# Kernel optimization log

Hardware: AMD Instinct MI355X
Metric: run time of the kernel (lower is better)

The kernel has to match this reference:

```python
import jax, jax.numpy as jnp
import numpy as np

B, N = 8, 2048
DIN, DS, DO, GE, HID = 2, 32, 32, 8, 32
CHEB_K = 3
N_SUPPORTS = 2
D_CAT = DIN + 2 * DS            # 66, input to the two AGCNs
D_BASIS = N_SUPPORTS * CHEB_K * D_CAT  # 396


def setup_inputs() -> dict:
    key = jax.random.key(0)
    ks = jax.random.split(key, 12)
    xt = jax.random.normal(ks[0], (B, N, DIN), dtype=jnp.float32)
    state1 = jax.random.normal(ks[1], (B, N, DS), dtype=jnp.float32)
    state2 = jax.random.normal(ks[2], (B, N, DS), dtype=jnp.float32)
    gatembedding = jax.random.normal(ks[3], (B, N, GE), dtype=jnp.float32)
    # adaptive adjacency supports: row-stochastic (softmax over neighbors), 2 supports
    supports = jax.nn.softmax(jax.random.normal(ks[4], (N_SUPPORTS, B, N, N), dtype=jnp.float32), axis=-1)

    def xavier(k, shape):
        fan_in, fan_out = shape[0], shape[1]
        std = float(np.sqrt(2.0 / (fan_in + fan_out)))
        return jax.random.normal(k, shape, dtype=jnp.float32) * std

    return {
        "xt": xt, "state1": state1, "state2": state2,
        "gatembedding": gatembedding, "supports": supports,
        "mlp_w": xavier(ks[5], (DIN + 2 * DS + GE, DO)), "mlp_b": jnp.zeros((DO,), jnp.float32),
        "gate_w": xavier(ks[6], (D_BASIS, 3 * DO)), "gate_b": jnp.zeros((3 * DO,), jnp.float32),
        "upd_w": xavier(ks[7], (D_BASIS, DO)), "upd_b": jnp.zeros((DO,), jnp.float32),
        "hop_w": xavier(ks[8], (DO, HID)), "hop_b": jnp.zeros((HID,), jnp.float32),
    }


def _agcn(x, supports, W, b):
    """Chebyshev graph conv: for each support, basis T0=I, T1=A, Tk=2A Tk-1 - Tk-2,
    applied to x (linearity lets us recurse on T_k @ x directly, same math)."""
    terms = []
    for i in range(N_SUPPORTS):  # fixed small structural loop
        A = supports[i]                                  # [B,N,N]
        t_prev, t_cur = x, jnp.einsum('bnm,bmc->bnc', A, x)
        ts = [t_prev, t_cur]
        for _ in range(2, CHEB_K):
            t_prev, t_cur = t_cur, 2.0 * jnp.einsum('bnm,bmc->bnc', A, t_cur) - t_prev
            ts.append(t_cur)
        terms.extend(ts)
    x_g = jnp.concatenate(terms, axis=-1)                # [B,N,2*K*c]
    return jnp.einsum('bni,io->bno', x_g, W) + b


def reference(xt, state1, state2, gatembedding, supports,
              mlp_w, mlp_b, gate_w, gate_b, upd_w, upd_b, hop_w, hop_b):
    # MLP mixing gate between the two incoming states
    gate_in = jnp.concatenate([xt, state1, state2, gatembedding], axis=-1)
    mr = jax.nn.sigmoid(gate_in @ mlp_w + mlp_b)
    state = mr * state1 + (1.0 - mr) * state2
    # graph-conv GRU gates
    X = jnp.concatenate([xt, state1, state2], axis=-1)   # [B,N,DIN+2*DS]
    zz_r = jax.nn.sigmoid(_agcn(X, supports, gate_w, gate_b))
    z1, z2, r = zz_r[..., :DO], zz_r[..., DO:2 * DO], zz_r[..., 2 * DO:]
    candidate = jnp.concatenate([xt, z1 * state1, z2 * state2], axis=-1)
    hc = jnp.tanh(_agcn(candidate, supports, upd_w, upd_b))
    h = r * state + (1.0 - r) * hc                        # [B,N,DO]
    transnext = h @ hop_w + hop_b                         # [B,N,HID]
    return (h, transnext)
```

## Files before the change

### kernel.cpp

```cpp
#include <hip/hip_runtime.h>

#define NN 2048
#define BB 8
#define KT 416
#define SLOT (80 * NN)

typedef __bf16 bf16;
typedef __bf16 bf16x4 __attribute__((ext_vector_type(4)));
typedef __bf16 bf16x8 __attribute__((ext_vector_type(8)));
typedef float  f32x4  __attribute__((ext_vector_type(4)));

__device__ __forceinline__ void bar_lgkm() {
    asm volatile("s_waitcnt lgkmcnt(0)" ::: "memory");
    __builtin_amdgcn_s_barrier();
}

__global__ void prep_weights(const float* __restrict__ gw, const float* __restrict__ uw,
                             bf16* __restrict__ Wg, bf16* __restrict__ Wu)
{
    int i = blockIdx.x * 256 + threadIdx.x;
    if (i < 96 * KT) {
        int o = i / KT, k = i % KT, t = k / 80, c = k % 80;
        float v = 0.0f;
        if (c < 66) {
            if (t == 0)      v = gw[c*96+o] - gw[(132+c)*96+o] + gw[(198+c)*96+o] - gw[(330+c)*96+o];
            else if (t == 1) v = gw[(66+c)*96+o];
            else if (t == 2) v = 2.0f * gw[(132+c)*96+o];
            else if (t == 3) v = gw[(264+c)*96+o];
            else             v = 2.0f * gw[(330+c)*96+o];
        }
        Wg[i] = (bf16)v;
    }
    if (i < 32 * KT) {
        int o = i / KT, k = i % KT, t = k / 80, c = k % 80;
        float v = 0.0f;
        if (c < 66) {
            if (t == 0)      v = uw[c*32+o] - uw[(132+c)*32+o] + uw[(198+c)*32+o] - uw[(330+c)*32+o];
            else if (t == 1) v = uw[(66+c)*32+o];
            else if (t == 2) v = 2.0f * uw[(132+c)*32+o];
            else if (t == 3) v = uw[(264+c)*32+o];
            else             v = 2.0f * uw[(330+c)*32+o];
        }
        Wu[i] = (bf16)v;
    }
}

__global__ __launch_bounds__(256)
void prep_nodes(const float* __restrict__ xt, const float* __restrict__ s1,
                const float* __restrict__ s2, const float* __restrict__ ge,
                const float* __restrict__ mlp_w, const float* __restrict__ mlp_b,
                float* __restrict__ state, bf16* __restrict__ T)
{
    __shared__ float wl[74 * 32];
    __shared__ float bl[32];
    __shared__ __align__(16) float statel[64][36];
    __shared__ __align__(16) bf16  Xl[80][72];
    const int tid = threadIdx.x;

    for (int i = tid; i < 592; i += 256) ((float4*)wl)[i] = ((const float4*)mlp_w)[i];
    if (tid < 32) bl[tid] = mlp_b[tid];
    {
        int bb = blockIdx.x >> 5, chunk = blockIdx.x & 31;
        uint2* dst = (uint2*)((char*)T + ((size_t)bb * KT * NN + 400 * NN) * 2 + (size_t)chunk * 2048);
        dst[tid] = make_uint2(0u, 0u);
    }
    for (int i = tid; i < 14 * 64; i += 256) Xl[66 + (i >> 6)][i & 63] = (bf16)0.0f;
    __syncthreads();

    const int nl = tid & 63, og = tid >> 6, o0 = og * 8;
    const size_t node0 = (size_t)blockIdx.x * 64;
    const size_t node = node0 + nl;
    const int b = (int)(node0 >> 11);
    const int nb0 = (int)(node0 & 2047);
    const float* p1 = s1 + node * 32;
    const float* p2 = s2 + node * 32;
    const float* pg = ge + node * 8;

    float acc[8];
    #pragma unroll
    for (int j = 0; j < 8; ++j) acc[j] = bl[o0 + j];
    float2 px = *(const float2*)(xt + node * 2);
    #pragma unroll
    for (int j = 0; j < 8; ++j) acc[j] += px.x * wl[o0 + j] + px.y * wl[32 + o0 + j];

    float k1[8], k2[8];
    #pragma unroll
    for (int ii = 0; ii < 8; ++ii) {
        float4 v = *(const float4*)(p1 + ii * 4);
        const float* vp = (const float*)&v;
        if (ii == 2 * og)     { k1[0]=vp[0]; k1[1]=vp[1]; k1[2]=vp[2]; k1[3]=vp[3]; }
        if (ii == 2 * og + 1) { k1[4]=vp[0]; k1[5]=vp[1]; k1[6]=vp[2]; k1[7]=vp[3]; }
        #pragma unroll
        for (int p = 0; p < 4; ++p) {
            #pragma unroll
            for (int j = 0; j < 8; ++j) acc[j] += vp[p] * wl[(2 + ii*4 + p) * 32 + o0 + j];
        }
    }
    #pragma unroll
    for (int ii = 0; ii < 8; ++ii) {
        float4 v = *(const float4*)(p2 + ii * 4);
        const float* vp = (const float*)&v;
        if (ii == 2 * og)     { k2[0]=vp[0]; k2[1]=vp[1]; k2[2]=vp[2]; k2[3]=vp[3]; }
        if (ii == 2 * og + 1) { k2[4]=vp[0]; k2[5]=vp[1]; k2[6]=vp[2]; k2[7]=vp[3]; }
        #pragma unroll
        for (int p = 0; p < 4; ++p) {
            #pragma unroll
            for (int j = 0; j < 8; ++j) acc[j] += vp[p] * wl[(34 + ii*4 + p) * 32 + o0 + j];
        }
    }
    #pragma unroll
    for (int ii = 0; ii < 2; ++ii) {
        float4 v = *(const float4*)(pg + ii * 4);
        const float* vp = (const float*)&v;
        #pragma unroll
        for (int p = 0; p < 4; ++p) {
            #pragma unroll
            for (int j = 0; j < 8; ++j) acc[j] += vp[p] * wl[(66 + ii*4 + p) * 32 + o0 + j];
        }
    }
    #pragma unroll
    for (int j = 0; j < 8; ++j) {
        float mr = 1.0f / (1.0f + __expf(-acc[j]));
        statel[nl][o0 + j] = mr * k1[j] + (1.0f - mr) * k2[j];
        Xl[2 + o0 + j][nl]  = (bf16)k1[j];
        Xl[34 + o0 + j][nl] = (bf16)k2[j];
    }
    if (og == 0) { Xl[0][nl] = (bf16)px.x; Xl[1][nl] = (bf16)px.y; }
    __syncthreads();

    for (int i = tid; i < 512; i += 256) {
        int n_ = i >> 3, c = (i & 7) * 4;
        *(float4*)&state[node0 * 32 + n_ * 32 + c] = *(const float4*)&statel[n_][c];
    }
    bf16* Tb = T + (size_t)b * KT * NN;
    for (int i = tid; i < 640; i += 256) {
        int r = i >> 3, seg = i & 7;
        *(uint4*)(Tb + (size_t)r * NN + nb0 + seg * 8) = *(const uint4*)&Xl[r][seg * 8];
    }
}

template<int MODE>
__global__ __launch_bounds__(256, 2)
void gemm_cheb(const float* __restrict__ Aall, bf16* Abf, bf16* T,
               int in0, int in1, int out0, int out1)
{
    __shared__ __align__(16) bf16 lA[2][64][40];
    __shared__ __align__(16) bf16 lB[2][80][40];

    const int sb = blockIdx.y;
    const int s = sb >> 3, b = sb & 7;
    const int m0 = blockIdx.x * 64;
    const float* A = Aall + (size_t)sb * NN * NN + (size_t)m0 * NN;
    bf16* Ab = Abf + (size_t)sb * NN * NN + (size_t)m0 * NN;
    bf16* Tb = T + (size_t)b * KT * NN;
    const bf16* Bt = Tb + (size_t)(s ? in1 : in0) * SLOT;
    bf16*       Ct = Tb + (size_t)(s ? out1 : out0) * SLOT + m0;

    const int tid  = threadIdx.x;
    const int wave = tid >> 6;
    const int lane = tid & 63;

    const int arow = tid >> 3, aseg = tid & 7;
    const int arw2 = tid >> 2, asg2 = tid & 3;
    const int brow = tid >> 2, bseg = tid & 3;
    const int brow2 = 64 + (tid >> 2);

    float4 ra0A, ra1A, ra0B, ra1B;
    uint4  ra2A, ra2B;
    uint4  rb0A, rb1A, rb0B, rb1B;

    auto gload = [&](float4& xa0, float4& xa1, uint4& xa2, uint4& xb0, uint4& xb1, int k0) {
        if constexpr (MODE == 2) {
            xa2 = *(const uint4*)(Ab + (size_t)arw2 * NN + k0 + asg2 * 8);
        } else {
            xa0 = *(const float4*)(A + (size_t)arow * NN + k0 + aseg * 4);
            xa1 = *(const float4*)(A + (size_t)(arow + 32) * NN + k0 + aseg * 4);
        }
        xb0 = *(const uint4*)(Bt + (size_t)brow * NN + k0 + bseg * 8);
        if (tid < 64) xb1 = *(const uint4*)(Bt + (size_t)brow2 * NN + k0 + bseg * 8);
    };
    auto stage = [&](int buf, float4& xa0, float4& xa1, uint4& xa2, uint4& xb0, uint4& xb1, int k0) {
        if constexpr (MODE == 2) {
            *(uint4*)&lA[buf][arw2][asg2 * 8] = xa2;
        } else {
            bf16x4 a0, a1;
            a0[0]=(bf16)xa0.x; a0[1]=(bf16)xa0.y; a0[2]=(bf16)xa0.z; a0[3]=(bf16)xa0.w;
            a1[0]=(bf16)xa1.x; a1[1]=(bf16)xa1.y; a1[2]=(bf16)xa1.z; a1[3]=(bf16)xa1.w;
            *(bf16x4*)&lA[buf][arow][aseg * 4]      = a0;
            *(bf16x4*)&lA[buf][arow + 32][aseg * 4] = a1;
            if constexpr (MODE == 1) {
                *(bf16x4*)(Ab + (size_t)arow * NN + k0 + aseg * 4)        = a0;
                *(bf16x4*)(Ab + (size_t)(arow + 32) * NN + k0 + aseg * 4) = a1;
            }
        }
        *(uint4*)&lB[buf][brow][bseg * 8] = xb0;
        if (tid < 64) *(uint4*)&lB[buf][brow2][bseg * 8] = xb1;
    };

    f32x4 acc[5] = {};
    const int frow = lane & 15;
    const int fko  = (lane >> 4) * 8;

    auto compute = [&](int buf) {
        bf16x8 af = *(const bf16x8*)&lA[buf][wave * 16 + frow][fko];
        #pragma unroll
        for (int ct = 0; ct < 5; ++ct) {
            bf16x8 bv = *(const bf16x8*)&lB[buf][ct * 16 + frow][fko];
            acc[ct] = __builtin_amdgcn_mfma_f32_16x16x32_bf16(af, bv, acc[ct], 0, 0, 0);
        }
    };

    gload(ra0A, ra1A, ra2A, rb0A, rb1A, 0);
    gload(ra0B, ra1B, ra2B, rb0B, rb1B, 32);
    for (int kt = 0; kt < 64; kt += 2) {
        stage(0, ra0A, ra1A, ra2A, rb0A, rb1A, kt * 32);
        if (kt < 62) gload(ra0A, ra1A, ra2A, rb0A, rb1A, (kt + 2) * 32);
        bar_lgkm();
        compute(0);
        stage(1, ra0B, ra1B, ra2B, rb0B, rb1B, (kt + 1) * 32);
        if (kt < 61) gload(ra0B, ra1B, ra2B, rb0B, rb1B, (kt + 3) * 32);
        bar_lgkm();
        compute(1);
    }

    const int ccol = lane & 15;
    const int crow = (lane >> 4) * 4;
    #pragma unroll
    for (int ct = 0; ct < 5; ++ct) {
        bf16x4 o;
        o[0]=(bf16)acc[ct][0]; o[1]=(bf16)acc[ct][1]; o[2]=(bf16)acc[ct][2]; o[3]=(bf16)acc[ct][3];
        *(bf16x4*)&Ct[(size_t)(ct * 16 + ccol) * NN + wave * 16 + crow] = o;
    }
}

__global__ __launch_bounds__(256)
void proj_gate(const bf16* T, const bf16* __restrict__ Wg, const float* __restrict__ gate_b,
               const float* __restrict__ s1, const float* __restrict__ s2,
               bf16* Tmut, float* __restrict__ rT)
{
    __shared__ __align__(16) bf16 Wl[96][424];
    __shared__ __align__(16) bf16 Bl[2][64][44];
    const int b = blockIdx.y, n0 = blockIdx.x * 64, tid = threadIdx.x;
    const bf16* Tb = T + (size_t)b * KT * NN;

    for (int i = tid; i < 96 * 52; i += 256) {
        int r = i / 52, seg = i % 52;
        *(uint4*)&Wl[r][seg * 8] = *(const uint4*)(Wg + (size_t)r * KT + seg * 8);
    }
    const int kk = tid >> 3, seg = tid & 7;
    uint4 rbA, rbB;
    auto gloadv = [&](uint4& r, int k0) { r = *(const uint4*)(Tb + (size_t)(k0 + kk) * NN + n0 + seg * 8); };
    auto scat = [&](int buf, uint4& r) {
        bf16 tmp[8]; *(uint4*)tmp = r;
        #pragma unroll
        for (int j = 0; j < 8; ++j) Bl[buf][seg * 8 + j][kk] = tmp[j];
    };
    const int lane = tid & 63, wave = tid >> 6;
    const int fr = lane & 15, qd = lane >> 4;

    f32x4 acc[6] = {};
    auto comp = [&](int buf, int st) {
        bf16x8 bv = *(const bf16x8*)&Bl[buf][wave * 16 + fr][qd * 8];
        #pragma unroll
        for (int f = 0; f < 6; ++f) {
            bf16x8 av = *(const bf16x8*)&Wl[f * 16 + fr][st * 32 + qd * 8];
            acc[f] = __builtin_amdgcn_mfma_f32_16x16x32_bf16(av, bv, acc[f], 0, 0, 0);
        }
    };

    gloadv(rbA, 0); gloadv(rbB, 32);
    for (int st = 0; st < 12; st += 2) {
        scat(0, rbA);
        gloadv(rbA, (st + 2) * 32);
        bar_lgkm();
        comp(0, st);
        scat(1, rbB);
        if (st < 10) gloadv(rbB, (st + 3) * 32);
        bar_lgkm();
        comp(1, st + 1);
    }
    scat(0, rbA);
    bar_lgkm();
    comp(0, 12);

    const int nn = n0 + wave * 16 + fr;
    const size_t node = (size_t)b * NN + nn;
    bf16* Cd = Tmut + (size_t)b * KT * NN;
    #pragma unroll
    for (int f = 0; f < 6; ++f) {
        const int o0 = f * 16 + qd * 4;
        float4 gb4 = *(const float4*)(gate_b + o0);
        const float* gb = (const float*)&gb4;
        float sg[4];
        #pragma unroll
        for (int r = 0; r < 4; ++r) sg[r] = 1.0f / (1.0f + __expf(-(acc[f][r] + gb[r])));
        if (f < 2) {
            float4 sv4 = *(const float4*)(s1 + node * 32 + o0);
            const float* sv = (const float*)&sv4;
            #pragma unroll
            for (int r = 0; r < 4; ++r) Cd[(size_t)(2 + o0 + r) * NN + nn] = (bf16)(sg[r] * sv[r]);
        } else if (f < 4) {
            const int oo = o0 - 32;
            float4 sv4 = *(const float4*)(s2 + node * 32 + oo);
            const float* sv = (const float*)&sv4;
            #pragma unroll
            for (int r = 0; r < 4; ++r) Cd[(size_t)(34 + oo + r) * NN + nn] = (bf16)(sg[r] * sv[r]);
        } else {
            const int oo = o0 - 64;
            #pragma unroll
            for (int r = 0; r < 4; ++r) rT[((size_t)b * 32 + oo + r) * NN + nn] = sg[r];
        }
    }
}

__global__ __launch_bounds__(256)
void proj_upd(const bf16* __restrict__ T, const bf16* __restrict__ Wu,
              const float* __restrict__ upd_b, const float* __restrict__ state,
              const float* __restrict__ rT, const float* __restrict__ hop_w,
              const float* __restrict__ hop_b, float* __restrict__ out)
{
    __shared__ __align__(16) bf16 Wl[32][424];
    __shared__ __align__(16) bf16 Bl[2][64][44];
    __shared__ __align__(16) float hsh[64][36];
    __shared__ float hw[1024];
    const int b = blockIdx.y, n0 = blockIdx.x * 64, tid = threadIdx.x;
    const bf16* Tb = T + (size_t)b * KT * NN;

    for (int i = tid; i < 32 * 52; i += 256) {
        int r = i / 52, seg = i % 52;
        *(uint4*)&Wl[r][seg * 8] = *(const uint4*)(Wu + (size_t)r * KT + seg * 8);
    }
    for (int i = tid; i < 256; i += 256) ((float4*)hw)[i] = ((const float4*)hop_w)[i];
    const int kk = tid >> 3, seg = tid & 7;
    uint4 rbA, rbB;
    auto gloadv = [&](uint4& r, int k0) { r = *(const uint4*)(Tb + (size_t)(k0 + kk) * NN + n0 + seg * 8); };
    auto scat = [&](int buf, uint4& r) {
        bf16 tmp[8]; *(uint4*)tmp = r;
        #pragma unroll
        for (int j = 0; j < 8; ++j) Bl[buf][seg * 8 + j][kk] = tmp[j];
    };
    const int lane = tid & 63, wave = tid >> 6;
    const int fr = lane & 15, qd = lane >> 4;

    f32x4 acc[2] = {};
    auto comp = [&](int buf, int st) {
        bf16x8 bv = *(const bf16x8*)&Bl[buf][wave * 16 + fr][qd * 8];
        #pragma unroll
        for (int f = 0; f < 2; ++f) {
            bf16x8 av = *(const bf16x8*)&Wl[f * 16 + fr][st * 32 + qd * 8];
            acc[f] = __builtin_amdgcn_mfma_f32_16x16x32_bf16(av, bv, acc[f], 0, 0, 0);
        }
    };

    gloadv(rbA, 0); gloadv(rbB, 32);
    for (int st = 0; st < 12; st += 2) {
        scat(0, rbA);
        gloadv(rbA, (st + 2) * 32);
        bar_lgkm();
        comp(0, st);
        scat(1, rbB);
        if (st < 10) gloadv(rbB, (st + 3) * 32);
        bar_lgkm();
        comp(1, st + 1);
    }
    scat(0, rbA);
    bar_lgkm();
    comp(0, 12);

    const int nn = n0 + wave * 16 + fr;
    const size_t node = (size_t)b * NN + nn;
    const int nl = wave * 16 + fr;
    #pragma unroll
    for (int f = 0; f < 2; ++f) {
        const int o0 = f * 16 + qd * 4;
        float4 ub4 = *(const float4*)(upd_b + o0);
        const float* ub = (const float*)&ub4;
        float4 st4 = *(const float4*)(state + node * 32 + o0);
        const float* sv = (const float*)&st4;
        #pragma unroll
        for (int r = 0; r < 4; ++r) {
            const int o = o0 + r;
            float hc = tanhf(acc[f][r] + ub[r]);
            float rv = rT[((size_t)b * 32 + o) * NN + nn];
            hsh[nl][o] = rv * sv[r] + (1.0f - rv) * hc;
        }
    }
    __syncthreads();

    const int nl2 = tid & 63, og = tid >> 6;
    const size_t node2 = (size_t)b * NN + n0 + nl2;
    float tac[8];
    #pragma unroll
    for (int j = 0; j < 8; ++j) tac[j] = hop_b[og * 8 + j];
    #pragma unroll
    for (int kc = 0; kc < 8; ++kc) {
        float4 hv4 = *(const float4*)&hsh[nl2][kc * 4];
        const float* hv = (const float*)&hv4;
        #pragma unroll
        for (int p = 0; p < 4; ++p) {
            #pragma unroll
            for (int j = 0; j < 8; ++j) tac[j] += hv[p] * hw[(kc * 4 + p) * 32 + og * 8 + j];
        }
    }
    float* out2 = out + (size_t)BB * NN * 32;
    *(float4*)&out[node2 * 32 + og * 8]     = *(const float4*)&hsh[nl2][og * 8];
    *(float4*)&out[node2 * 32 + og * 8 + 4] = *(const float4*)&hsh[nl2][og * 8 + 4];
    float4 t0; float* t0p = (float*)&t0;
    t0p[0]=tac[0]; t0p[1]=tac[1]; t0p[2]=tac[2]; t0p[3]=tac[3];
    *(float4*)&out2[node2 * 32 + og * 8] = t0;
    t0p[0]=tac[4]; t0p[1]=tac[5]; t0p[2]=tac[6]; t0p[3]=tac[7];
    *(float4*)&out2[node2 * 32 + og * 8 + 4] = t0;
}

extern "C" void kernel_launch(void* const* d_in, const int* in_sizes, int n_in,
                              void* d_out, int out_size, void* d_ws, size_t ws_size,
                              hipStream_t stream)
{
    const float* xt     = (const float*)d_in[0];
    const float* s1     = (const float*)d_in[1];
    const float* s2     = (const float*)d_in[2];
    const float* ge     = (const float*)d_in[3];
    const float* sup    = (const float*)d_in[4];
    const float* mlp_w  = (const float*)d_in[5];
    const float* mlp_b  = (const float*)d_in[6];
    const float* gate_w = (const float*)d_in[7];
    const float* gate_b = (const float*)d_in[8];
    const float* upd_w  = (const float*)d_in[9];
    const float* upd_b  = (const float*)d_in[10];
    const float* hop_w  = (const float*)d_in[11];
    const float* hop_b  = (const float*)d_in[12];
    float* out = (float*)d_out;

    char* ws = (char*)d_ws;
    size_t off = 0;
    auto alloc = [&](size_t bytes) -> void* {
        void* p = ws + off;
        off += (bytes + 255) & ~(size_t)255;
        return p;
    };
    bf16*  T     = (bf16*) alloc((size_t)BB * KT * NN * 2);
    float* state = (float*)alloc((size_t)BB * NN * 32 * 4);
    float* rT    = (float*)alloc((size_t)BB * 32 * NN * 4);
    bf16*  Wg    = (bf16*) alloc((size_t)96 * KT * 2);
    bf16*  Wu    = (bf16*) alloc((size_t)32 * KT * 2);
    bf16*  Abf   = (bf16*) (ws + off);
    const bool useA = (off + (size_t)16 * NN * NN * 2) <= ws_size;

    prep_weights<<<156, 256, 0, stream>>>(gate_w, upd_w, Wg, Wu);
    prep_nodes<<<256, 256, 0, stream>>>(xt, s1, s2, ge, mlp_w, mlp_b, state, T);

    if (useA) {
        gemm_cheb<1><<<dim3(32, 16), 256, 0, stream>>>(sup, Abf, T, 0, 0, 1, 3);
        gemm_cheb<2><<<dim3(32, 16), 256, 0, stream>>>(sup, Abf, T, 1, 3, 2, 4);
        proj_gate<<<dim3(32, 8), 256, 0, stream>>>(T, Wg, gate_b, s1, s2, T, rT);
        gemm_cheb<2><<<dim3(32, 16), 256, 0, stream>>>(sup, Abf, T, 0, 0, 1, 3);
        gemm_cheb<2><<<dim3(32, 16), 256, 0, stream>>>(sup, Abf, T, 1, 3, 2, 4);
    } else {
        gemm_cheb<0><<<dim3(32, 16), 256, 0, stream>>>(sup, Abf, T, 0, 0, 1, 3);
        gemm_cheb<0><<<dim3(32, 16), 256, 0, stream>>>(sup, Abf, T, 1, 3, 2, 4);
        proj_gate<<<dim3(32, 8), 256, 0, stream>>>(T, Wg, gate_b, s1, s2, T, rT);
        gemm_cheb<0><<<dim3(32, 16), 256, 0, stream>>>(sup, Abf, T, 0, 0, 1, 3);
        gemm_cheb<0><<<dim3(32, 16), 256, 0, stream>>>(sup, Abf, T, 1, 3, 2, 4);
    }
    proj_upd<<<dim3(32, 8), 256, 0, stream>>>(T, Wu, upd_b, state, rT, hop_w, hop_b, out);
}
```

Measured before the change: 586.3 us.

## Load A fragments directly into registers and double K step per stage

```diff
diff --git a/kernel.cpp b/kernel.cpp
--- a/kernel.cpp
+++ b/kernel.cpp
@@ -144,8 +144,7 @@
 void gemm_cheb(const float* __restrict__ Aall, bf16* Abf, bf16* T,
                int in0, int in1, int out0, int out1)
 {
-    __shared__ __align__(16) bf16 lA[2][64][40];
-    __shared__ __align__(16) bf16 lB[2][80][40];
+    __shared__ __align__(16) bf16 lB[2][2][80][40];
 
     const int sb = blockIdx.y;
     const int s = sb >> 3, b = sb & 7;
@@ -159,68 +158,99 @@
     const int tid  = threadIdx.x;
     const int wave = tid >> 6;
     const int lane = tid & 63;
-
-    const int arow = tid >> 3, aseg = tid & 7;
-    const int arw2 = tid >> 2, asg2 = tid & 3;
-    const int brow = tid >> 2, bseg = tid & 3;
-    const int brow2 = 64 + (tid >> 2);
-
-    float4 ra0A, ra1A, ra0B, ra1B;
-    uint4  ra2A, ra2B;
-    uint4  rb0A, rb1A, rb0B, rb1B;
-
-    auto gload = [&](float4& xa0, float4& xa1, uint4& xa2, uint4& xb0, uint4& xb1, int k0) {
-        if constexpr (MODE == 2) {
-            xa2 = *(const uint4*)(Ab + (size_t)arw2 * NN + k0 + asg2 * 8);
-        } else {
-            xa0 = *(const float4*)(A + (size_t)arow * NN + k0 + aseg * 4);
-            xa1 = *(const float4*)(A + (size_t)(arow + 32) * NN + k0 + aseg * 4);
-        }
-        xb0 = *(const uint4*)(Bt + (size_t)brow * NN + k0 + bseg * 8);
-        if (tid < 64) xb1 = *(const uint4*)(Bt + (size_t)brow2 * NN + k0 + bseg * 8);
-    };
-    auto stage = [&](int buf, float4& xa0, float4& xa1, uint4& xa2, uint4& xb0, uint4& xb1, int k0) {
-        if constexpr (MODE == 2) {
-            *(uint4*)&lA[buf][arw2][asg2 * 8] = xa2;
-        } else {
-            bf16x4 a0, a1;
-            a0[0]=(bf16)xa0.x; a0[1]=(bf16)xa0.y; a0[2]=(bf16)xa0.z; a0[3]=(bf16)xa0.w;
-            a1[0]=(bf16)xa1.x; a1[1]=(bf16)xa1.y; a1[2]=(bf16)xa1.z; a1[3]=(bf16)xa1.w;
-            *(bf16x4*)&lA[buf][arow][aseg * 4]      = a0;
-            *(bf16x4*)&lA[buf][arow + 32][aseg * 4] = a1;
-            if constexpr (MODE == 1) {
-                *(bf16x4*)(Ab + (size_t)arow * NN + k0 + aseg * 4)        = a0;
-                *(bf16x4*)(Ab + (size_t)(arow + 32) * NN + k0 + aseg * 4) = a1;
-            }
-        }
-        *(uint4*)&lB[buf][brow][bseg * 8] = xb0;
-        if (tid < 64) *(uint4*)&lB[buf][brow2][bseg * 8] = xb1;
-    };
-
-    f32x4 acc[5] = {};
     const int frow = lane & 15;
     const int fko  = (lane >> 4) * 8;
-
-    auto compute = [&](int buf) {
-        bf16x8 af = *(const bf16x8*)&lA[buf][wave * 16 + frow][fko];
+    const int am   = wave * 16 + frow;
+
+    const float* Af = A  + (size_t)am * NN + fko;
+    const bf16*  Ap = Ab + (size_t)am * NN + fko;
+    bf16*        As = Ab + (size_t)am * NN + fko;
+
+    const int brow  = tid >> 2, bseg = tid & 3;
+    const int brow2 = 64 + (tid >> 2);
+
+    auto gloadB = [&](uint4& r0h0, uint4& r1h0, uint4& r0h1, uint4& r1h1, int k0) {
+        r0h0 = *(const uint4*)(Bt + (size_t)brow * NN + k0 + bseg * 8);
+        r0h1 = *(const uint4*)(Bt + (size_t)brow * NN + k0 + 32 + bseg * 8);
+        if (tid < 64) {
+            r1h0 = *(const uint4*)(Bt + (size_t)brow2 * NN + k0 + bseg * 8);
+            r1h1 = *(const uint4*)(Bt + (size_t)brow2 * NN + k0 + 32 + bseg * 8);
+        }
+    };
+    auto stageB = [&](int buf, uint4& r0h0, uint4& r1h0, uint4& r0h1, uint4& r1h1) {
+        *(uint4*)&lB[buf][0][brow][bseg * 8] = r0h0;
+        *(uint4*)&lB[buf][1][brow][bseg * 8] = r0h1;
+        if (tid < 64) {
+            *(uint4*)&lB[buf][0][brow2][bseg * 8] = r1h0;
+            *(uint4*)&lB[buf][1][brow2][bseg * 8] = r1h1;
+        }
+    };
+    auto gloadA = [&](uint4& h0, uint4& h1, float4& g00, float4& g01,
+                      float4& g10, float4& g11, int k0) {
+        if constexpr (MODE == 2) {
+            h0 = *(const uint4*)(Ap + k0);
+            h1 = *(const uint4*)(Ap + k0 + 32);
+        } else {
+            g00 = *(const float4*)(Af + k0);
+            g01 = *(const float4*)(Af + k0 + 4);
+            g10 = *(const float4*)(Af + k0 + 32);
+            g11 = *(const float4*)(Af + k0 + 36);
+        }
+    };
+    auto mkaf = [&](uint4& h, float4& g0, float4& g1, int k0) -> bf16x8 {
+        if constexpr (MODE == 2) {
+            return *(bf16x8*)&h;
+        } else {
+            bf16x8 r;
+            r[0]=(bf16)g0.x; r[1]=(bf16)g0.y; r[2]=(bf16)g0.z; r[3]=(bf16)g0.w;
+            r[4]=(bf16)g1.x; r[5]=(bf16)g1.y; r[6]=(bf16)g1.z; r[7]=(bf16)g1.w;
+            if constexpr (MODE == 1) *(bf16x8*)(As + k0) = r;
+            return r;
+        }
+    };
+
+    f32x4 acc[5] = {};
+    auto compute = [&](int buf, bf16x8 af0, bf16x8 af1) {
         #pragma unroll
         for (int ct = 0; ct < 5; ++ct) {
-            bf16x8 bv = *(const bf16x8*)&lB[buf][ct * 16 + frow][fko];
-            acc[ct] = __builtin_amdgcn_mfma_f32_16x16x32_bf16(af, bv, acc[ct], 0, 0, 0);
-        }
-    };
-
-    gload(ra0A, ra1A, ra2A, rb0A, rb1A, 0);
-    gload(ra0B, ra1B, ra2B, rb0B, rb1B, 32);
-    for (int kt = 0; kt < 64; kt += 2) {
-        stage(0, ra0A, ra1A, ra2A, rb0A, rb1A, kt * 32);
-        if (kt < 62) gload(ra0A, ra1A, ra2A, rb0A, rb1A, (kt + 2) * 32);
-        bar_lgkm();
-        compute(0);
-        stage(1, ra0B, ra1B, ra2B, rb0B, rb1B, (kt + 1) * 32);
-        if (kt < 61) gload(ra0B, ra1B, ra2B, rb0B, rb1B, (kt + 3) * 32);
-        bar_lgkm();
-        compute(1);
+            bf16x8 bv = *(const bf16x8*)&lB[buf][0][ct * 16 + frow][fko];
+            acc[ct] = __builtin_amdgcn_mfma_f32_16x16x32_bf16(af0, bv, acc[ct], 0, 0, 0);
+        }
+        #pragma unroll
+        for (int ct = 0; ct < 5; ++ct) {
+            bf16x8 bv = *(const bf16x8*)&lB[buf][1][ct * 16 + frow][fko];
+            acc[ct] = __builtin_amdgcn_mfma_f32_16x16x32_bf16(af1, bv, acc[ct], 0, 0, 0);
+        }
+    };
+
+    uint4 b00A, b10A, b01A, b11A, b00B, b10B, b01B, b11B;
+    uint4 a0A, a1A, a0B, a1B;
+    float4 f00A, f01A, f10A, f11A, f00B, f01B, f10B, f11B;
+
+    gloadB(b00A, b10A, b01A, b11A, 0);
+    gloadB(b00B, b10B, b01B, b11B, 64);
+    gloadA(a0A, a1A, f00A, f01A, f10A, f11A, 0);
+    gloadA(a0B, a1B, f00B, f01B, f10B, f11B, 64);
+
+    for (int it = 0; it < 32; it += 2) {
+        stageB(0, b00A, b10A, b01A, b11A);
+        bf16x8 e0 = mkaf(a0A, f00A, f01A, it * 64);
+        bf16x8 e1 = mkaf(a1A, f10A, f11A, it * 64 + 32);
+        if (it < 30) {
+            gloadB(b00A, b10A, b01A, b11A, (it + 2) * 64);
+            gloadA(a0A, a1A, f00A, f01A, f10A, f11A, (it + 2) * 64);
+        }
+        bar_lgkm();
+        compute(0, e0, e1);
+        stageB(1, b00B, b10B, b01B, b11B);
+        bf16x8 o0 = mkaf(a0B, f00B, f01B, (it + 1) * 64);
+        bf16x8 o1 = mkaf(a1B, f10B, f11B, (it + 1) * 64 + 32);
+        if (it < 29) {
+            gloadB(b00B, b10B, b01B, b11B, (it + 3) * 64);
+            gloadA(a0B, a1B, f00B, f01B, f10B, f11B, (it + 3) * 64);
+        }
+        bar_lgkm();
+        compute(1, o0, o1);
     }
 
     const int ccol = lane & 15;
```

New measurement: 548.7 us. 6.4% less time.

## Load GEMM operands straight into registers, skipping LDS, and pre-convert supports in a separate kernel

Applied to the files above, without the earlier changes.

```diff
diff --git a/kernel.cpp b/kernel.cpp
--- a/kernel.cpp
+++ b/kernel.cpp
@@ -46,6 +46,22 @@
 }
 
 __global__ __launch_bounds__(256)
+void a2bf(const float* __restrict__ s, bf16* __restrict__ d)
+{
+    const float4* s4 = (const float4*)s;
+    uint4* d4 = (uint4*)d;
+    const size_t n8 = (size_t)16 * NN * NN / 8;
+    for (size_t i = (size_t)blockIdx.x * 256 + threadIdx.x; i < n8;
+         i += (size_t)gridDim.x * 256) {
+        float4 u = s4[2 * i], v = s4[2 * i + 1];
+        bf16x8 r;
+        r[0]=(bf16)u.x; r[1]=(bf16)u.y; r[2]=(bf16)u.z; r[3]=(bf16)u.w;
+        r[4]=(bf16)v.x; r[5]=(bf16)v.y; r[6]=(bf16)v.z; r[7]=(bf16)v.w;
+        d4[i] = *(uint4*)&r;
+    }
+}
+
+__global__ __launch_bounds__(256)
 void prep_nodes(const float* __restrict__ xt, const float* __restrict__ s1,
                 const float* __restrict__ s2, const float* __restrict__ ge,
                 const float* __restrict__ mlp_w, const float* __restrict__ mlp_b,
@@ -139,88 +155,72 @@
     }
 }
 
-template<int MODE>
+template<int F32>
 __global__ __launch_bounds__(256, 2)
-void gemm_cheb(const float* __restrict__ Aall, bf16* Abf, bf16* T,
-               int in0, int in1, int out0, int out1)
-{
-    __shared__ __align__(16) bf16 lA[2][64][40];
-    __shared__ __align__(16) bf16 lB[2][80][40];
-
+void gemm_direct(const float* __restrict__ Aall, const bf16* __restrict__ Abf,
+                 bf16* __restrict__ T, int in0, int in1, int out0, int out1)
+{
     const int sb = blockIdx.y;
     const int s = sb >> 3, b = sb & 7;
     const int m0 = blockIdx.x * 64;
-    const float* A = Aall + (size_t)sb * NN * NN + (size_t)m0 * NN;
-    bf16* Ab = Abf + (size_t)sb * NN * NN + (size_t)m0 * NN;
+    const int tid = threadIdx.x, wave = tid >> 6, lane = tid & 63;
+    const int frow = lane & 15, fko = (lane >> 4) * 8;
+    const int am = m0 + wave * 16 + frow;
+
     bf16* Tb = T + (size_t)b * KT * NN;
     const bf16* Bt = Tb + (size_t)(s ? in1 : in0) * SLOT;
     bf16*       Ct = Tb + (size_t)(s ? out1 : out0) * SLOT + m0;
-
-    const int tid  = threadIdx.x;
-    const int wave = tid >> 6;
-    const int lane = tid & 63;
-
-    const int arow = tid >> 3, aseg = tid & 7;
-    const int arw2 = tid >> 2, asg2 = tid & 3;
-    const int brow = tid >> 2, bseg = tid & 3;
-    const int brow2 = 64 + (tid >> 2);
-
-    float4 ra0A, ra1A, ra0B, ra1B;
-    uint4  ra2A, ra2B;
-    uint4  rb0A, rb1A, rb0B, rb1B;
-
-    auto gload = [&](float4& xa0, float4& xa1, uint4& xa2, uint4& xb0, uint4& xb1, int k0) {
-        if constexpr (MODE == 2) {
-            xa2 = *(const uint4*)(Ab + (size_t)arw2 * NN + k0 + asg2 * 8);
+    const bf16*  Ap = Abf + (size_t)sb * NN * NN + (size_t)am * NN + fko;
+    const float* Af = Aall + (size_t)sb * NN * NN + (size_t)am * NN + fko;
+    const bf16*  Bp = Bt + (size_t)frow * NN + fko;
+
+    f32x4 acc[5] = {};
+
+    uint4 aA0, aA1, aB0, aB1;
+    float4 gA[4], gB[4];
+    uint4 bbA[5][2], bbB[5][2];
+
+    auto ld = [&](uint4& a0, uint4& a1, float4 (&g)[4], uint4 (&bb)[5][2], int k0) {
+        if constexpr (F32) {
+            g[0] = *(const float4*)(Af + k0);
+            g[1] = *(const float4*)(Af + k0 + 4);
+            g[2] = *(const float4*)(Af + k0 + 32);
+            g[3] = *(const float4*)(Af + k0 + 36);
         } else {
-            xa0 = *(const float4*)(A + (size_t)arow * NN + k0 + aseg * 4);
-            xa1 = *(const float4*)(A + (size_t)(arow + 32) * NN + k0 + aseg * 4);
-        }
-        xb0 = *(const uint4*)(Bt + (size_t)brow * NN + k0 + bseg * 8);
-        if (tid < 64) xb1 = *(const uint4*)(Bt + (size_t)brow2 * NN + k0 + bseg * 8);
-    };
-    auto stage = [&](int buf, float4& xa0, float4& xa1, uint4& xa2, uint4& xb0, uint4& xb1, int k0) {
-        if constexpr (MODE == 2) {
-            *(uint4*)&lA[buf][arw2][asg2 * 8] = xa2;
-        } else {
-            bf16x4 a0, a1;
-            a0[0]=(bf16)xa0.x; a0[1]=(bf16)xa0.y; a0[2]=(bf16)xa0.z; a0[3]=(bf16)xa0.w;
-            a1[0]=(bf16)xa1.x; a1[1]=(bf16)xa1.y; a1[2]=(bf16)xa1.z; a1[3]=(bf16)xa1.w;
-            *(bf16x4*)&lA[buf][arow][aseg * 4]      = a0;
-            *(bf16x4*)&lA[buf][arow + 32][aseg * 4] = a1;
-            if constexpr (MODE == 1) {
-                *(bf16x4*)(Ab + (size_t)arow * NN + k0 + aseg * 4)        = a0;
-                *(bf16x4*)(Ab + (size_t)(arow + 32) * NN + k0 + aseg * 4) = a1;
-            }
-        }
-        *(uint4*)&lB[buf][brow][bseg * 8] = xb0;
-        if (tid < 64) *(uint4*)&lB[buf][brow2][bseg * 8] = xb1;
-    };
-
-    f32x4 acc[5] = {};
-    const int frow = lane & 15;
-    const int fko  = (lane >> 4) * 8;
-
-    auto compute = [&](int buf) {
-        bf16x8 af = *(const bf16x8*)&lA[buf][wave * 16 + frow][fko];
+            a0 = *(const uint4*)(Ap + k0);
+            a1 = *(const uint4*)(Ap + k0 + 32);
+        }
         #pragma unroll
         for (int ct = 0; ct < 5; ++ct) {
-            bf16x8 bv = *(const bf16x8*)&lB[buf][ct * 16 + frow][fko];
-            acc[ct] = __builtin_amdgcn_mfma_f32_16x16x32_bf16(af, bv, acc[ct], 0, 0, 0);
-        }
-    };
-
-    gload(ra0A, ra1A, ra2A, rb0A, rb1A, 0);
-    gload(ra0B, ra1B, ra2B, rb0B, rb1B, 32);
-    for (int kt = 0; kt < 64; kt += 2) {
-        stage(0, ra0A, ra1A, ra2A, rb0A, rb1A, kt * 32);
-        if (kt < 62) gload(ra0A, ra1A, ra2A, rb0A, rb1A, (kt + 2) * 32);
-        bar_lgkm();
-        compute(0);
-        stage(1, ra0B, ra1B, ra2B, rb0B, rb1B, (kt + 1) * 32);
-        if (kt < 61) gload(ra0B, ra1B, ra2B, rb0B, rb1B, (kt + 3) * 32);
-        bar_lgkm();
-        compute(1);
+            bb[ct][0] = *(const uint4*)(Bp + (size_t)ct * 16 * NN + k0);
+            bb[ct][1] = *(const uint4*)(Bp + (size_t)ct * 16 * NN + k0 + 32);
+        }
+    };
+    auto cv = [&](float4 g0, float4 g1) -> bf16x8 {
+        bf16x8 r;
+        r[0]=(bf16)g0.x; r[1]=(bf16)g0.y; r[2]=(bf16)g0.z; r[3]=(bf16)g0.w;
+        r[4]=(bf16)g1.x; r[5]=(bf16)g1.y; r[6]=(bf16)g1.z; r[7]=(bf16)g1.w;
+        return r;
+    };
+    auto comp = [&](uint4& a0, uint4& a1, float4 (&g)[4], uint4 (&bb)[5][2]) {
+        bf16x8 af0, af1;
+        if constexpr (F32) { af0 = cv(g[0], g[1]); af1 = cv(g[2], g[3]); }
+        else { af0 = *(bf16x8*)&a0; af1 = *(bf16x8*)&a1; }
+        #pragma unroll
+        for (int ct = 0; ct < 5; ++ct)
+            acc[ct] = __builtin_amdgcn_mfma_f32_16x16x32_bf16(af0, *(bf16x8*)&bb[ct][0], acc[ct], 0, 0, 0);
+        #pragma unroll
+        for (int ct = 0; ct < 5; ++ct)
+            acc[ct] = __builtin_amdgcn_mfma_f32_16x16x32_bf16(af1, *(bf16x8*)&bb[ct][1], acc[ct], 0, 0, 0);
+    };
+
+    ld(aA0, aA1, gA, bbA, 0);
+    ld(aB0, aB1, gB, bbB, 64);
+    for (int it = 0; it < 32; it += 2) {
+        comp(aA0, aA1, gA, bbA);
+        if (it < 30) ld(aA0, aA1, gA, bbA, (it + 2) * 64);
+        comp(aB0, aB1, gB, bbB);
+        if (it < 29) ld(aB0, aB1, gB, bbB, (it + 3) * 64);
     }
 
     const int ccol = lane & 15;
@@ -447,20 +447,21 @@
     const bool useA = (off + (size_t)16 * NN * NN * 2) <= ws_size;
 
     prep_weights<<<156, 256, 0, stream>>>(gate_w, upd_w, Wg, Wu);
+    if (useA) a2bf<<<2048, 256, 0, stream>>>(sup, Abf);
     prep_nodes<<<256, 256, 0, stream>>>(xt, s1, s2, ge, mlp_w, mlp_b, state, T);
 
     if (useA) {
-        gemm_cheb<1><<<dim3(32, 16), 256, 0, stream>>>(sup, Abf, T, 0, 0, 1, 3);
-        gemm_cheb<2><<<dim3(32, 16), 256, 0, stream>>>(sup, Abf, T, 1, 3, 2, 4);
+        gemm_direct<0><<<dim3(32, 16), 256, 0, stream>>>(sup, Abf, T, 0, 0, 1, 3);
+        gemm_direct<0><<<dim3(32, 16), 256, 0, stream>>>(sup, Abf, T, 1, 3, 2, 4);
         proj_gate<<<dim3(32, 8), 256, 0, stream>>>(T, Wg, gate_b, s1, s2, T, rT);
-        gemm_cheb<2><<<dim3(32, 16), 256, 0, stream>>>(sup, Abf, T, 0, 0, 1, 3);
-        gemm_cheb<2><<<dim3(32, 16), 256, 0, stream>>>(sup, Abf, T, 1, 3, 2, 4);
+        gemm_direct<0><<<dim3(32, 16), 256, 0, stream>>>(sup, Abf, T, 0, 0, 1, 3);
+        gemm_direct<0><<<dim3(32, 16), 256, 0, stream>>>(sup, Abf, T, 1, 3, 2, 4);
     } else {
-        gemm_cheb<0><<<dim3(32, 16), 256, 0, stream>>>(sup, Abf, T, 0, 0, 1, 3);
-        gemm_cheb<0><<<dim3(32, 16), 256, 0, stream>>>(sup, Abf, T, 1, 3, 2, 4);
+        gemm_direct<1><<<dim3(32, 16), 256, 0, stream>>>(sup, Abf, T, 0, 0, 1, 3);
+        gemm_direct<1><<<dim3(32, 16), 256, 0, stream>>>(sup, Abf, T, 1, 3, 2, 4);
         proj_gate<<<dim3(32, 8), 256, 0, stream>>>(T, Wg, gate_b, s1, s2, T, rT);
-        gemm_cheb<0><<<dim3(32, 16), 256, 0, stream>>>(sup, Abf, T, 0, 0, 1, 3);
-        gemm_cheb<0><<<dim3(32, 16), 256, 0, stream>>>(sup, Abf, T, 1, 3, 2, 4);
+        gemm_direct<1><<<dim3(32, 16), 256, 0, stream>>>(sup, Abf, T, 0, 0, 1, 3);
+        gemm_direct<1><<<dim3(32, 16), 256, 0, stream>>>(sup, Abf, T, 1, 3, 2, 4);
     }
     proj_upd<<<dim3(32, 8), 256, 0, stream>>>(T, Wu, upd_b, state, rT, hop_w, hop_b, out);
 }
```

Result: slower. 781.9 us (+33.3%).
